# Kernel tuning notes

Hardware: AMD Instinct MI355X
Metric: run time of the kernel (lower is better)

Reference implementation:

```python
import jax, jax.numpy as jnp
import numpy as np

N, E, D, H, DK, T, R, KN, KR = 50000, 800000, 128, 8, 16, 3, 4, 2, 2

def setup_inputs() -> dict:
    key = jax.random.key(0)
    ks = jax.random.split(key, 16)
    lin_s = np.sqrt(1.0 / D).astype(np.float32)   # ~ nn.Linear init scale
    glo_s = np.sqrt(2.0 / (DK + DK)).astype(np.float32)  # glorot for [*,H,DK,DK]
    return {
        'x': jax.random.normal(ks[0], (N, D), jnp.float32),
        'Wk': jax.random.normal(ks[1], (KN, D, D), jnp.float32) * lin_s,
        'bk': jnp.zeros((KN, D), jnp.float32),
        'Wq': jax.random.normal(ks[2], (KN, D, D), jnp.float32) * lin_s,
        'bq': jnp.zeros((KN, D), jnp.float32),
        'Wv': jax.random.normal(ks[3], (KN, D, D), jnp.float32) * lin_s,
        'bv': jnp.zeros((KN, D), jnp.float32),
        'rel_pri': jnp.ones((KR, H), jnp.float32),
        'rel_att': jax.random.normal(ks[4], (KR, H, DK, DK), jnp.float32) * glo_s,
        'rel_msg': jax.random.normal(ks[5], (KR, H, DK, DK), jnp.float32) * glo_s,
        'n_alpha': jax.random.normal(ks[6], (T, KN), jnp.float32) * 0.001,
        'r_alpha': jax.random.normal(ks[7], (R, KR), jnp.float32) * 0.001,
        'W_up': jax.random.normal(ks[8], (T, D, D), jnp.float32) * lin_s,
        'b_up': jnp.zeros((T, D), jnp.float32),
        'gamma': jnp.ones((T, D), jnp.float32),
        'beta': jnp.zeros((T, D), jnp.float32),
        'edge_index': jax.random.randint(ks[9], (2, E), 0, N),
        'node_type': jax.random.randint(ks[10], (N,), 0, T),
        'edge_type': jax.random.randint(ks[11], (E,), 0, R),
    }

def reference(x, Wk, bk, Wq, bq, Wv, bv, rel_pri, rel_att, rel_msg,
              n_alpha, r_alpha, W_up, b_up, gamma, beta,
              edge_index, node_type, edge_type):
    n, d = x.shape
    h = rel_att.shape[1]; dk = d // h
    n_types = W_up.shape[0]; n_rel = r_alpha.shape[0]
    # NAS-mixed per-node-type k/q/v linears
    an = jax.nn.softmax(n_alpha, axis=-1)[node_type]        # [N, KN]
    def mix(W, b):
        cand = jnp.einsum('nd,kdo->kno', x, W) + b[:, None, :]  # [KN, N, D]
        return jnp.einsum('kno,nk->no', cand, an).reshape(n, h, dk)
    k = mix(Wk, bk); q = mix(Wq, bq); v = mix(Wv, bv)
    # NAS-mixed per-relation bilinear att/msg and priority
    br = jax.nn.softmax(r_alpha, axis=-1)                   # [R, KR]
    att_r = jnp.einsum('rk,khde->rhde', br, rel_att)        # [R, H, DK, DK]
    msg_r = jnp.einsum('rk,khde->rhde', br, rel_msg)
    pri_r = br @ rel_pri                                    # [R, H]
    src, dst = edge_index[0], edge_index[1]
    k_e = k[src]; q_e = q[dst]; v_e = v[src]                # [E, H, DK]
    k_t = jnp.zeros_like(k_e); m_t = jnp.zeros_like(v_e)
    for r in range(n_rel):  # small fixed relation loop
        sel = (edge_type == r)[:, None, None]
        k_t = k_t + jnp.where(sel, jnp.einsum('ehd,hdo->eho', k_e, att_r[r]), 0.0)
        m_t = m_t + jnp.where(sel, jnp.einsum('ehd,hdo->eho', v_e, msg_r[r]), 0.0)
    score = (q_e * k_t).sum(-1) * pri_r[edge_type] / np.float32(np.sqrt(dk))  # [E, H]
    # segment softmax over destination nodes
    mx = jax.ops.segment_max(score, dst, num_segments=n)
    ex = jnp.exp(score - mx[dst])
    den = jax.ops.segment_sum(ex, dst, num_segments=n)
    w = ex / (den[dst] + 1e-16)                             # [E, H]
    out = jax.ops.segment_sum(m_t * w[..., None], dst, num_segments=n).reshape(n, d)
    # heterogeneous update: gelu -> per-type linear -> residual -> per-type LN
    res = jax.nn.gelu(out)
    trans = jnp.zeros_like(x)
    for t in range(n_types):
        sel = (node_type == t)[:, None]
        trans = trans + jnp.where(sel, res @ W_up[t] + b_up[t], 0.0)
    hres = trans + x
    mu = hres.mean(-1, keepdims=True)
    var = hres.var(-1, keepdims=True)
    hn = (hres - mu) / jnp.sqrt(var + 1e-5)
    return hn * gamma[node_type] + beta[node_type]
```

## Files before the change

### kernel.cpp

```cpp
#include <hip/hip_runtime.h>
#include <hip/hip_bf16.h>

#define DEV __device__ __forceinline__

using frag8 = __attribute__((ext_vector_type(8))) short;
using f32x4 = __attribute__((ext_vector_type(4))) float;

DEV float b2f(__hip_bfloat16 v){ return __bfloat162float(v); }
DEV __hip_bfloat16 f2b(float f){ return __float2bfloat16(f); }
DEV short f2s(float f){ __hip_bfloat16 h = __float2bfloat16(f); short s; __builtin_memcpy(&s,&h,2); return s; }
DEV float bflo(unsigned u){ unsigned x = u<<16; float f; __builtin_memcpy(&f,&x,4); return f; }
DEV float bfhi(unsigned u){ unsigned x = u&0xFFFF0000u; float f; __builtin_memcpy(&f,&x,4); return f; }
DEV unsigned packbf(float a, float b){
  return (unsigned)(unsigned short)f2s(a) | ((unsigned)(unsigned short)f2s(b)<<16);
}

DEV bool is_bf16_mode(const void* rel_pri){
  return ((const unsigned*)rel_pri)[0] == 0x3F803F80u;
}
DEV float ldf(const void* p, int i, bool isbf){
  return isbf ? __bfloat162float(((const __hip_bfloat16*)p)[i]) : ((const float*)p)[i];
}

struct PrepArgs {
  const void *Wk,*Wq,*Wv,*bk,*bq,*bv,*rel_pri,*rel_att,*rel_msg,*n_alpha,*r_alpha,*Wup,*bup,*gm,*bt;
  const int* ntype;
  float *anW,*priS,*bmix,*bqt,*upc;
  __hip_bfloat16 *bsw,*wsw,*mswz;
  int* count3;
  int N;
};

__global__ void k_prep(PrepArgs P){
  bool isbf = is_bf16_mode(P.rel_pri);
  float an[3][2], br[4][2];
  #pragma unroll
  for (int t=0;t<3;t++){
    float a0=ldf(P.n_alpha,t*2,isbf), a1=ldf(P.n_alpha,t*2+1,isbf);
    float m=fmaxf(a0,a1); float e0=__expf(a0-m), e1=__expf(a1-m); float inv=1.f/(e0+e1);
    an[t][0]=e0*inv; an[t][1]=e1*inv;
  }
  #pragma unroll
  for (int r=0;r<4;r++){
    float a0=ldf(P.r_alpha,r*2,isbf), a1=ldf(P.r_alpha,r*2+1,isbf);
    float m=fmaxf(a0,a1); float e0=__expf(a0-m), e1=__expf(a1-m); float inv=1.f/(e0+e1);
    br[r][0]=e0*inv; br[r][1]=e1*inv;
  }
  int g = blockIdx.x*blockDim.x + threadIdx.x;
  int stride = gridDim.x*blockDim.x;

  for (int idx=g; idx<196608; idx+=stride){
    int jj = idx&7, lane=(idx>>3)&63, s=(idx>>9)&3, tile=(idx>>11)&15, chunk=idx>>15;
    int k = s*32 + ((lane>>4)<<3) + jj;
    int col = tile*16 + (lane&15);
    int cand = col>>7, c = col&127;
    float v;
    if (chunk==0)      v = ldf(P.Wk, cand*16384 + k*128 + c, isbf);
    else if (chunk==1) v = ldf(P.Wv, cand*16384 + k*128 + c, isbf);
    else {
      int r = chunk-2, h = c>>4, d = c&15;
      float acc=0.f;
      #pragma unroll
      for (int o=0;o<16;o++){
        float att = br[r][0]*ldf(P.rel_att,(h*16+d)*16+o,isbf) + br[r][1]*ldf(P.rel_att,2048+(h*16+d)*16+o,isbf);
        acc += ldf(P.Wq, cand*16384 + k*128 + h*16+o, isbf) * att;
      }
      v = acc;
    }
    P.bsw[idx] = f2b(v);
  }
  for (int idx=g; idx<49152; idx+=stride){
    int t3 = idx>>14, f = idx&16383;
    int jj=f&7, lane=(f>>3)&63, s=(f>>9)&3, nt=f>>11;
    int k = s*32 + ((lane>>4)<<3)+jj;
    int cc = nt*16 + (lane&15);
    P.wsw[idx] = f2b(ldf(P.Wup, t3*16384 + k*128 + cc, isbf));
  }
  for (int idx=g; idx<65536; idx+=stride){
    int jj=idx&7, lane=(idx>>3)&63, s=(idx>>9)&3, tile=(idx>>11)&7, kc=idx>>14;
    int k = kc*128 + s*32 + ((lane>>4)<<3)+jj;
    int col = tile*16 + (lane&15);
    int r = k>>7, h=(k>>4)&7, d=k&15;
    int h2 = col>>4, o = col&15;
    float v = 0.f;
    if (h2==h)
      v = br[r][0]*ldf(P.rel_msg,(h*16+d)*16+o,isbf) + br[r][1]*ldf(P.rel_msg,2048+(h*16+d)*16+o,isbf);
    P.mswz[idx] = f2b(v);
  }
  for (int idx=g; idx<768; idx+=stride){
    int mat = idx/384, rem = idx - mat*384, t = rem>>7, c = rem&127;
    const void* b = mat==0 ? P.bk : P.bv;
    P.bmix[idx] = an[t][0]*ldf(b,c,isbf) + an[t][1]*ldf(b,128+c,isbf);
  }
  for (int idx=g; idx<1536; idx+=stride){
    int t = idx>>9, rem = idx&511, r = rem>>7, c = rem&127;
    int h = c>>4, d = c&15;
    float acc=0.f;
    #pragma unroll
    for (int o=0;o<16;o++){
      float att = br[r][0]*ldf(P.rel_att,(h*16+d)*16+o,isbf) + br[r][1]*ldf(P.rel_att,2048+(h*16+d)*16+o,isbf);
      float bqm = an[t][0]*ldf(P.bq,h*16+o,isbf) + an[t][1]*ldf(P.bq,128+h*16+o,isbf);
      acc += bqm*att;
    }
    P.bqt[idx] = acc;
  }
  for (int idx=g; idx<1152; idx+=stride){
    int p = idx/384, rem = idx - p*384;
    const void* src = p==0 ? P.bup : p==1 ? P.gm : P.bt;
    P.upc[idx] = ldf(src, rem, isbf);
  }
  for (int idx=g; idx<32; idx+=stride){
    int r = idx>>3, h = idx&7;
    P.priS[idx] = 0.25f*(br[r][0]*ldf(P.rel_pri,h,isbf) + br[r][1]*ldf(P.rel_pri,8+h,isbf));
  }
  for (int idx=g; idx<6; idx+=stride) P.anW[idx] = an[idx>>1][idx&1];
  {
    int c0=0, c1=0, c2=0;
    for (int idx=g; idx<P.N; idx+=stride){
      int t = P.ntype[idx];
      c0 += (t==0); c1 += (t==1); c2 += (t==2);
    }
    #pragma unroll
    for (int m=1; m<64; m<<=1){
      c0 += __shfl_xor(c0, m, 64);
      c1 += __shfl_xor(c1, m, 64);
      c2 += __shfl_xor(c2, m, 64);
    }
    if ((threadIdx.x & 63) == 0){
      if (c0) atomicAdd(&P.count3[0], c0);
      if (c1) atomicAdd(&P.count3[1], c1);
      if (c2) atomicAdd(&P.count3[2], c2);
    }
  }
}

__global__ __launch_bounds__(256) void k_xcast(const void* __restrict__ x, const void* __restrict__ relp,
                                               __hip_bfloat16* __restrict__ xb, int total8){
  if (is_bf16_mode(relp)) return;
  int p = blockIdx.x*256 + threadIdx.x;
  if (p >= total8) return;
  const float4* xf = reinterpret_cast<const float4*>(x) + (size_t)p*2;
  float4 u = xf[0], v = xf[1];
  frag8 r;
  r[0]=f2s(u.x); r[1]=f2s(u.y); r[2]=f2s(u.z); r[3]=f2s(u.w);
  r[4]=f2s(v.x); r[5]=f2s(v.y); r[6]=f2s(v.z); r[7]=f2s(v.w);
  *reinterpret_cast<frag8*>(xb + (size_t)p*8) = r;
}

__global__ void k_hist(const int* __restrict__ eidx, int* __restrict__ count, int E){
  int e = blockIdx.x*256 + threadIdx.x;
  if (e < E) atomicAdd(&count[eidx[E+e]], 1);
}

__global__ __launch_bounds__(1024) void k_scan1(const int* __restrict__ count, int* __restrict__ excl,
                                                int* __restrict__ ctot, int N){
  __shared__ int s[1024];
  int i = blockIdx.x*1024 + threadIdx.x;
  int v = (i < N) ? count[i] : 0;
  s[threadIdx.x] = v;
  __syncthreads();
  int run = v;
  for (int off=1; off<1024; off<<=1){
    int add = (threadIdx.x >= off) ? s[threadIdx.x - off] : 0;
    __syncthreads();
    run += add; s[threadIdx.x] = run;
    __syncthreads();
  }
  if (i < N) excl[i] = run - v;
  if (threadIdx.x == 1023) ctot[blockIdx.x] = run;
}

__global__ void k_scan2(const int* __restrict__ ctot, int* __restrict__ coff,
                        const int* __restrict__ c3, int* __restrict__ segp, int NC){
  if (threadIdx.x==0 && blockIdx.x==0){
    int run=0;
    for (int c=0;c<NC;c++){ coff[c]=run; run+=ctot[c]; }
    int a0 = (c3[0]+127)&~127;
    int a1 = (c3[1]+127)&~127;
    int a2 = (c3[2]+127)&~127;
    segp[0]=0; segp[1]=a0; segp[2]=a0+a1; segp[3]=a0+a1+a2;
  }
}

__global__ __launch_bounds__(256) void k_nscatter(const int* __restrict__ ntype, const int* __restrict__ segp,
                           int* __restrict__ cur3, int* __restrict__ nlist, int N){
  __shared__ int wcnt[4][3];
  __shared__ int tbase[3];
  int tid = threadIdx.x;
  int n = blockIdx.x*256 + tid;
  int w = tid>>6, lane = tid&63;
  int t = (n < N) ? ntype[n] : -1;
  unsigned long long b0 = __ballot(t==0);
  unsigned long long b1 = __ballot(t==1);
  unsigned long long b2 = __ballot(t==2);
  if (lane==0){
    wcnt[w][0] = __popcll(b0);
    wcnt[w][1] = __popcll(b1);
    wcnt[w][2] = __popcll(b2);
  }
  __syncthreads();
  if (tid < 3){
    int c = wcnt[0][tid]+wcnt[1][tid]+wcnt[2][tid]+wcnt[3][tid];
    tbase[tid] = c ? atomicAdd(&cur3[tid], c) : 0;
  }
  __syncthreads();
  if (t >= 0){
    unsigned long long mask = t==0?b0 : t==1?b1 : b2;
    int lanerank = __popcll(mask & ((1ULL<<lane)-1ULL));
    int waveoff = 0;
    #pragma unroll
    for (int ww=0; ww<4; ww++) if (ww < w) waveoff += wcnt[ww][t];
    nlist[segp[t] + tbase[t] + waveoff + lanerank] = n;
  }
}

__global__ void k_escatter(const int* __restrict__ eidx, const int* __restrict__ etype,
                           const int* __restrict__ coff, const int* __restrict__ excl,
                           int* __restrict__ cursor, int* __restrict__ pack, int E){
  int e = blockIdx.x*256 + threadIdx.x;
  if (e < E){
    int src = eidx[e];
    int dst = eidx[E+e];
    int rt  = etype[e];
    int pos = coff[dst>>10] + excl[dst] + atomicAdd(&cursor[dst], 1);
    pack[pos] = src | (rt<<20);
  }
}

__global__ __launch_bounds__(256) void k_qkvqt(
    const void* __restrict__ x, const __hip_bfloat16* __restrict__ xb,
    const int* __restrict__ ntype,
    const void* __restrict__ relp,
    const __hip_bfloat16* __restrict__ bsw, const float* __restrict__ anW,
    const float* __restrict__ bmix, const float* __restrict__ bqt,
    __hip_bfloat16* __restrict__ kb, __hip_bfloat16* __restrict__ vb,
    __hip_bfloat16* __restrict__ qtb, int N, int perx)
{
  __shared__ __hip_bfloat16 Bs[16384];
  bool isbf = is_bf16_mode(relp);
  int tid = threadIdx.x;
  int w = tid>>6, lane = tid&63;
  int m16 = lane&15, q4 = lane>>4;

  int nrb = (N+127)>>7;
  int xcd  = blockIdx.x & 7;
  int slot = blockIdx.x >> 3;
  int lrb  = slot/12;
  int sub  = slot - lrb*12;
  int rb   = xcd*perx + lrb;
  if (rb >= nrb) return;
  int chunk = sub >> 1;
  int hh    = sub & 1;
  int base  = rb*128;

  const int4* bsw4 = reinterpret_cast<const int4*>(bsw) + chunk*4096;
  int4* Bs4 = reinterpret_cast<int4*>(Bs);
  #pragma unroll
  for (int u=0;u<8;u++){
    int srcT = 4*hh + (u&3) + ((u>>2)<<3);
    __builtin_amdgcn_global_load_lds(
        (const __attribute__((address_space(1))) void*)(bsw4 + srcT*256 + tid),
        (__attribute__((address_space(3))) void*)(Bs4 + u*256 + tid),
        16, 0, 0);
  }

  const __hip_bfloat16* xs = isbf ? (const __hip_bfloat16*)x : xb;
  frag8 a0[4], a1[4];
  {
    int rr0 = base + w*32 + m16;
    int rr1 = rr0 + 16;
    int r0 = rr0 < N ? rr0 : N-1;
    int r1 = rr1 < N ? rr1 : N-1;
    #pragma unroll
    for (int s=0;s<4;s++){
      a0[s] = *reinterpret_cast<const frag8*>(xs + (size_t)r0*128 + q4*8 + s*32);
      a1[s] = *reinterpret_cast<const frag8*>(xs + (size_t)r1*128 + q4*8 + s*32);
    }
  }
  int rowid[8]; float e0[8], e1[8]; int tt8[8];
  #pragma unroll
  for (int u=0;u<8;u++){
    int rs = u>>2, i = u&3;
    int rr = base + w*32 + rs*16 + q4*4 + i;
    rowid[u] = rr;
    int rc = rr < N ? rr : N-1;
    int t = ntype[rc]; tt8[u] = t;
    e0[u] = anW[t*2]; e1[u] = anW[t*2+1];
  }
  __syncthreads();
  const frag8* Bf = reinterpret_cast<const frag8*>(Bs);
  #pragma unroll
  for (int p=0;p<4;p++){
    f32x4 c00={0,0,0,0}, c01={0,0,0,0}, c10={0,0,0,0}, c11={0,0,0,0};
    #pragma unroll
    for (int s=0;s<4;s++){
      frag8 b0 = Bf[(p*4+s)*64 + lane];
      frag8 b1 = Bf[((p+4)*4+s)*64 + lane];
      c00 = __builtin_amdgcn_mfma_f32_16x16x32_bf16(a0[s], b0, c00, 0,0,0);
      c01 = __builtin_amdgcn_mfma_f32_16x16x32_bf16(a1[s], b0, c01, 0,0,0);
      c10 = __builtin_amdgcn_mfma_f32_16x16x32_bf16(a0[s], b1, c10, 0,0,0);
      c11 = __builtin_amdgcn_mfma_f32_16x16x32_bf16(a1[s], b1, c11, 0,0,0);
    }
    int c = (4*hh + p)*16 + m16;
    #pragma unroll
    for (int u=0;u<8;u++){
      int rs = u>>2, i = u&3;
      int rr = rowid[u];
      if (rr < N){
        float v0 = rs ? c01[i] : c00[i];
        float v1 = rs ? c11[i] : c10[i];
        float val = e0[u]*v0 + e1[u]*v1;
        if (chunk < 2){
          val += bmix[(chunk*3 + tt8[u])*128 + c];
          (chunk==0 ? kb : vb)[(size_t)rr*128 + c] = f2b(val);
        } else {
          int r = chunk-2;
          val += bqt[(tt8[u]*4 + r)*128 + c];
          qtb[(size_t)rr*512 + r*128 + c] = f2b(val);
        }
      }
    }
  }
}

__global__ __launch_bounds__(256) void k_aggr(
  const __hip_bfloat16* __restrict__ kb, const __hip_bfloat16* __restrict__ vb,
  const __hip_bfloat16* __restrict__ qtb,
  const int* __restrict__ count, const int* __restrict__ excl, const int* __restrict__ coff,
  const int* __restrict__ pack, const float* __restrict__ priS,
  __hip_bfloat16* __restrict__ accb, float* __restrict__ denb, int N)
{
  int w = threadIdx.x>>6, lane = threadIdx.x&63;
  int n = blockIdx.x*4 + w; if (n >= N) return;
  const unsigned* kb32 = (const unsigned*)kb;
  const unsigned* vb32 = (const unsigned*)vb;
  int h = lane>>3;
  float qx[4], qy[4], ps[4];
  {
    const unsigned* qrow = (const unsigned*)qtb + (size_t)n*256;
    #pragma unroll
    for (int r=0;r<4;r++){
      unsigned u = qrow[r*64 + lane];
      qx[r] = bflo(u); qy[r] = bfhi(u);
      ps[r] = priS[r*8 + h];
    }
  }
  int start = coff[n>>10] + excl[n];
  int deg = count[n];
  float ax0=0.f,ay0=0.f,ax1=0.f,ay1=0.f,ax2=0.f,ay2=0.f,ax3=0.f,ay3=0.f,den=0.f;

  for (int b0=0; b0<deg; b0+=64){
    int m = deg - b0; if (m > 64) m = 64;
    int pk = (lane < m) ? pack[start + b0 + lane] : 0;
    int pe = __builtin_amdgcn_readfirstlane(__shfl(pk, 0, 64));
    int rt = (pe>>20)&3, src = pe & 0xFFFFF;
    unsigned kw = kb32[(size_t)src*64 + lane];
    unsigned vw = vb32[(size_t)src*64 + lane];
    for (int i=0; i<m; i++){
      unsigned kc=kw, vc=vw; int rc=rt;
      if (i+1 < m){
        int pn = __builtin_amdgcn_readfirstlane(__shfl(pk, i+1, 64));
        rt = (pn>>20)&3; int s2 = pn & 0xFFFFF;
        kw = kb32[(size_t)s2*64 + lane];
        vw = vb32[(size_t)s2*64 + lane];
      }
      float k0=bflo(kc), k1=bfhi(kc), v0=bflo(vc), v1=bfhi(vc);
      float qxr, qyr, psr;
      if (rc==0){qxr=qx[0];qyr=qy[0];psr=ps[0];}
      else if (rc==1){qxr=qx[1];qyr=qy[1];psr=ps[1];}
      else if (rc==2){qxr=qx[2];qyr=qy[2];psr=ps[2];}
      else {qxr=qx[3];qyr=qy[3];psr=ps[3];}
      float prod = k0*qxr + k1*qyr;
      prod += __shfl_xor(prod, 1, 8);
      prod += __shfl_xor(prod, 2, 8);
      prod += __shfl_xor(prod, 4, 8);
      float ex = __expf(fminf(prod*psr, 30.f));
      den += ex;
      float e0 = ex*v0, e1 = ex*v1;
      if (rc==0){ax0+=e0; ay0+=e1;}
      else if (rc==1){ax1+=e0; ay1+=e1;}
      else if (rc==2){ax2+=e0; ay2+=e1;}
      else {ax3+=e0; ay3+=e1;}
    }
  }
  unsigned* arow = (unsigned*)accb + (size_t)n*256;
  arow[lane]       = packbf(ax0, ay0);
  arow[64 + lane]  = packbf(ax1, ay1);
  arow[128 + lane] = packbf(ax2, ay2);
  arow[192 + lane] = packbf(ax3, ay3);
  if ((lane&7)==0) denb[(size_t)n*8 + h] = den;
}

__global__ __launch_bounds__(256) void k_msgup(
  const __hip_bfloat16* __restrict__ accb, const float* __restrict__ denb,
  const void* __restrict__ x, const void* __restrict__ relp,
  const int* __restrict__ nlist, const int* __restrict__ segp,
  const __hip_bfloat16* __restrict__ mswz, const __hip_bfloat16* __restrict__ wsw,
  const float* __restrict__ upc, void* __restrict__ out, int N)
{
  __shared__ __hip_bfloat16 Ms[16384];
  __shared__ __hip_bfloat16 resS[128*136];
  bool isbf = is_bf16_mode(relp);
  int tid=threadIdx.x, w=tid>>6, lane=tid&63, m16=lane&15, q4=lane>>4;
  int pos0 = blockIdx.x*128;
  int sg1 = segp[1], sg2 = segp[2];
  int t = (pos0 >= sg2) ? 2 : (pos0 >= sg1) ? 1 : 0;

  int nA[2];
  #pragma unroll
  for (int rs=0; rs<2; rs++){
    int nid = nlist[pos0 + w*32 + rs*16 + m16];
    nA[rs] = nid < 0 ? 0 : nid;
  }
  int nC[8];
  #pragma unroll
  for (int u=0;u<8;u++){
    int rs=u>>2, i=u&3;
    nC[u] = nlist[pos0 + w*32 + rs*16 + q4*4 + i];
  }
  f32x4 c0[8], c1[8];
  #pragma unroll
  for (int nt=0;nt<8;nt++){ c0[nt]={0,0,0,0}; c1[nt]={0,0,0,0}; }
  const int4* msw4 = reinterpret_cast<const int4*>(mswz);
  int4* Ms4 = reinterpret_cast<int4*>(Ms);
  for (int kc=0; kc<4; kc++){
    __syncthreads();
    #pragma unroll
    for (int u=0;u<8;u++) Ms4[u*256+tid] = msw4[kc*2048 + u*256 + tid];
    __syncthreads();
    const frag8* Bf = reinterpret_cast<const frag8*>(Ms);
    frag8 a0[4], a1[4];
    #pragma unroll
    for (int s=0;s<4;s++){
      a0[s] = *reinterpret_cast<const frag8*>(accb + (size_t)nA[0]*512 + kc*128 + s*32 + q4*8);
      a1[s] = *reinterpret_cast<const frag8*>(accb + (size_t)nA[1]*512 + kc*128 + s*32 + q4*8);
    }
    #pragma unroll
    for (int s=0;s<4;s++){
      #pragma unroll
      for (int nt=0;nt<8;nt++){
        frag8 b = Bf[(nt*4+s)*64 + lane];
        c0[nt] = __builtin_amdgcn_mfma_f32_16x16x32_bf16(a0[s], b, c0[nt], 0,0,0);
        c1[nt] = __builtin_amdgcn_mfma_f32_16x16x32_bf16(a1[s], b, c1[nt], 0,0,0);
      }
    }
  }
  #pragma unroll
  for (int u=0;u<8;u++){
    int rs=u>>2, i=u&3;
    int rr = w*32 + rs*16 + q4*4 + i;
    int nid = nC[u]; int nc = nid<0?0:nid;
    #pragma unroll
    for (int nt=0;nt<8;nt++){
      float den = denb[(size_t)nc*8 + nt];
      float vv = (rs ? c1[nt][i] : c0[nt][i]) / (den + 1e-16f);
      float gl = 0.5f*vv*(1.f + tanhf(0.7978845608028654f*(vv + 0.044715f*vv*vv*vv)));
      resS[rr*136 + nt*16 + m16] = f2b(gl);
    }
  }
  __syncthreads();
  const int4* wsw4 = reinterpret_cast<const int4*>(wsw);
  #pragma unroll
  for (int u=0;u<8;u++) Ms4[u*256+tid] = wsw4[t*2048 + u*256 + tid];
  __syncthreads();
  f32x4 d0[8], d1[8];
  #pragma unroll
  for (int nt=0;nt<8;nt++){ d0[nt]={0,0,0,0}; d1[nt]={0,0,0,0}; }
  const frag8* Bf2 = reinterpret_cast<const frag8*>(Ms);
  #pragma unroll
  for (int s=0;s<4;s++){
    frag8 a0 = *reinterpret_cast<const frag8*>(&resS[(w*32 + m16)*136 + s*32 + q4*8]);
    frag8 a1 = *reinterpret_cast<const frag8*>(&resS[(w*32 + 16 + m16)*136 + s*32 + q4*8]);
    #pragma unroll
    for (int nt=0;nt<8;nt++){
      frag8 b = Bf2[(nt*4+s)*64 + lane];
      d0[nt] = __builtin_amdgcn_mfma_f32_16x16x32_bf16(a0, b, d0[nt], 0,0,0);
      d1[nt] = __builtin_amdgcn_mfma_f32_16x16x32_bf16(a1, b, d1[nt], 0,0,0);
    }
  }
  #pragma unroll
  for (int u=0;u<8;u++){
    int rs=u>>2, i=u&3;
    int nid = nC[u]; int nc = nid<0?0:nid;
    float hv[8], s1=0.f, s2=0.f;
    #pragma unroll
    for (int nt=0;nt<8;nt++){
      int col = nt*16+m16;
      float xr = isbf ? b2f(((const __hip_bfloat16*)x)[(size_t)nc*128+col])
                      : ((const float*)x)[(size_t)nc*128+col];
      float v = (rs ? d1[nt][i] : d0[nt][i]) + upc[t*128+col] + xr;
      hv[nt]=v; s1+=v; s2+=v*v;
    }
    #pragma unroll
    for (int mm=1; mm<16; mm<<=1){ s1 += __shfl_xor(s1, mm, 16); s2 += __shfl_xor(s2, mm, 16); }
    float mu = s1*(1.f/128.f);
    float var = s2*(1.f/128.f) - mu*mu;
    float rcp = rsqrtf(var + 1e-5f);
    if (nid >= 0){
      #pragma unroll
      for (int nt=0;nt<8;nt++){
        int col = nt*16+m16;
        float o = (hv[nt]-mu)*rcp*upc[384 + t*128+col] + upc[768 + t*128+col];
        if (isbf) ((__hip_bfloat16*)out)[(size_t)nid*128+col] = f2b(o);
        else      ((float*)out)[(size_t)nid*128+col] = o;
      }
    }
  }
}

extern "C" void kernel_launch(void* const* d_in, const int* in_sizes, int n_in,
                              void* d_out, int out_size, void* d_ws, size_t ws_size,
                              hipStream_t stream)
{
  const int* eidx  = (const int*)d_in[16];
  const int* ntype = (const int*)d_in[17];
  const int* etype = (const int*)d_in[18];

  const int N  = in_sizes[0]/128;
  const int E  = in_sizes[18];
  const int NC = (N + 1023)/1024;

  char* ws = (char*)d_ws;
  size_t off = 0;
  auto alloc = [&](size_t bytes){ size_t o = off; off += (bytes + 255) & ~(size_t)255; return o; };
  size_t o_count = alloc((size_t)N*4);
  size_t o_cursor= alloc((size_t)N*4);
  size_t o_c3    = alloc(16);
  size_t o_cur3  = alloc(16);
  size_t zbytes  = off;
  size_t o_nlist = alloc((size_t)(N+1024)*4);
  size_t o_excl  = alloc((size_t)N*4);
  size_t o_ctot  = alloc(256);
  size_t o_coff  = alloc(256);
  size_t o_segp  = alloc(16);
  size_t o_an    = alloc(6*4);
  size_t o_pri   = alloc(32*4);
  size_t o_bmix  = alloc(768*4);
  size_t o_bqt   = alloc(1536*4);
  size_t o_upc   = alloc(1152*4);
  size_t o_bsw   = alloc(196608*2);
  size_t o_wsw   = alloc(49152*2);
  size_t o_msw   = alloc(65536*2);
  size_t o_pack  = alloc((size_t)E*4);
  size_t o_xb    = alloc((size_t)N*128*2);
  size_t o_kb    = alloc((size_t)N*128*2);
  size_t o_vb    = alloc((size_t)N*128*2);
  size_t o_qt    = alloc((size_t)N*512*2);
  size_t o_acc   = alloc((size_t)N*512*2);
  size_t o_den   = alloc((size_t)N*8*4);
  (void)ws_size; (void)n_in; (void)out_size;

  hipMemsetAsync(ws, 0, zbytes, stream);
  hipMemsetAsync(ws + o_nlist, 0xFF, (size_t)(N+1024)*4, stream);

  PrepArgs P;
  P.Wk=d_in[1]; P.bk=d_in[2]; P.Wq=d_in[3]; P.bq=d_in[4]; P.Wv=d_in[5]; P.bv=d_in[6];
  P.rel_pri=d_in[7]; P.rel_att=d_in[8]; P.rel_msg=d_in[9];
  P.n_alpha=d_in[10]; P.r_alpha=d_in[11]; P.Wup=d_in[12]; P.bup=d_in[13]; P.gm=d_in[14]; P.bt=d_in[15];
  P.ntype=ntype;
  P.anW=(float*)(ws+o_an); P.priS=(float*)(ws+o_pri);
  P.bmix=(float*)(ws+o_bmix); P.bqt=(float*)(ws+o_bqt); P.upc=(float*)(ws+o_upc);
  P.bsw=(__hip_bfloat16*)(ws+o_bsw); P.wsw=(__hip_bfloat16*)(ws+o_wsw);
  P.mswz=(__hip_bfloat16*)(ws+o_msw);
  P.count3=(int*)(ws+o_c3); P.N=N;
  k_prep<<<512, 256, 0, stream>>>(P);

  int total8 = N*16;
  k_xcast<<<(total8+255)/256, 256, 0, stream>>>(d_in[0], d_in[7], (__hip_bfloat16*)(ws+o_xb), total8);

  k_hist<<<(E+255)/256, 256, 0, stream>>>(eidx, (int*)(ws+o_count), E);
  k_scan1<<<NC, 1024, 0, stream>>>((const int*)(ws+o_count), (int*)(ws+o_excl), (int*)(ws+o_ctot), N);
  k_scan2<<<1, 64, 0, stream>>>((const int*)(ws+o_ctot), (int*)(ws+o_coff),
                                (const int*)(ws+o_c3), (int*)(ws+o_segp), NC);
  k_nscatter<<<(N+255)/256, 256, 0, stream>>>(ntype, (const int*)(ws+o_segp),
                                              (int*)(ws+o_cur3), (int*)(ws+o_nlist), N);
  k_escatter<<<(E+255)/256, 256, 0, stream>>>(eidx, etype, (const int*)(ws+o_coff),
                                              (const int*)(ws+o_excl), (int*)(ws+o_cursor),
                                              (int*)(ws+o_pack), E);
  int nrb  = (N + 127)/128;
  int perx = (nrb + 7)/8;
  k_qkvqt<<<perx*12*8, 256, 0, stream>>>(d_in[0], (const __hip_bfloat16*)(ws+o_xb), ntype, d_in[7],
                                           (const __hip_bfloat16*)(ws+o_bsw),
                                           (const float*)(ws+o_an), (const float*)(ws+o_bmix),
                                           (const float*)(ws+o_bqt),
                                           (__hip_bfloat16*)(ws+o_kb), (__hip_bfloat16*)(ws+o_vb),
                                           (__hip_bfloat16*)(ws+o_qt), N, perx);
  k_aggr<<<(N+3)/4, 256, 0, stream>>>((const __hip_bfloat16*)(ws+o_kb), (const __hip_bfloat16*)(ws+o_vb),
                                (const __hip_bfloat16*)(ws+o_qt),
                                (const int*)(ws+o_count), (const int*)(ws+o_excl),
                                (const int*)(ws+o_coff), (const int*)(ws+o_pack),
                                (const float*)(ws+o_pri),
                                (__hip_bfloat16*)(ws+o_acc), (float*)(ws+o_den), N);
  int gUp = (N + 508)/128;
  k_msgup<<<gUp, 256, 0, stream>>>((const __hip_bfloat16*)(ws+o_acc), (const float*)(ws+o_den),
                                   d_in[0], d_in[7],
                                   (const int*)(ws+o_nlist), (const int*)(ws+o_segp),
                                   (const __hip_bfloat16*)(ws+o_msw), (const __hip_bfloat16*)(ws+o_wsw),
                                   (const float*)(ws+o_upc), d_out, N);
}
```

Before: 427.4 us.

## Precompute per-relation value messages per node and simplify edge aggregation

```diff
diff --git a/kernel.cpp b/kernel.cpp
--- a/kernel.cpp
+++ b/kernel.cpp
@@ -22,11 +22,23 @@
   return isbf ? __bfloat162float(((const __hip_bfloat16*)p)[i]) : ((const float*)p)[i];
 }
 
+#if __has_builtin(__builtin_amdgcn_fdot2_f32_bf16)
+typedef __bf16 bf16x2 __attribute__((ext_vector_type(2)));
+DEV float dot2b(unsigned a, unsigned b, float c){
+  bf16x2 av, bv; __builtin_memcpy(&av,&a,4); __builtin_memcpy(&bv,&b,4);
+  return __builtin_amdgcn_fdot2_f32_bf16(av, bv, c, false);
+}
+#else
+DEV float dot2b(unsigned a, unsigned b, float c){
+  return c + bflo(a)*bflo(b) + bfhi(a)*bfhi(b);
+}
+#endif
+
 struct PrepArgs {
-  const void *Wk,*Wq,*Wv,*bk,*bq,*bv,*rel_pri,*rel_att,*rel_msg,*n_alpha,*r_alpha,*Wup,*bup,*gm,*bt;
+  const void *x,*Wk,*Wq,*Wv,*bk,*bq,*bv,*rel_pri,*rel_att,*rel_msg,*n_alpha,*r_alpha,*Wup,*bup,*gm,*bt;
   const int* ntype;
-  float *anW,*priS,*bmix,*bqt,*upc;
-  __hip_bfloat16 *bsw,*wsw,*mswz;
+  float *anW,*priS,*bmixK,*bqt,*bvm,*upc;
+  __hip_bfloat16 *bsw,*wsw,*msw2,*xb;
   int* count3;
   int N;
 };
@@ -48,6 +60,17 @@
   }
   int g = blockIdx.x*blockDim.x + threadIdx.x;
   int stride = gridDim.x*blockDim.x;
+
+  if (!isbf){
+    const float4* xf = (const float4*)P.x;
+    for (int idx=g; idx<P.N*16; idx+=stride){
+      float4 u = xf[(size_t)idx*2], v = xf[(size_t)idx*2+1];
+      frag8 r;
+      r[0]=f2s(u.x); r[1]=f2s(u.y); r[2]=f2s(u.z); r[3]=f2s(u.w);
+      r[4]=f2s(v.x); r[5]=f2s(v.y); r[6]=f2s(v.z); r[7]=f2s(v.w);
+      *reinterpret_cast<frag8*>(P.xb + (size_t)idx*8) = r;
+    }
+  }
 
   for (int idx=g; idx<196608; idx+=stride){
     int jj = idx&7, lane=(idx>>3)&63, s=(idx>>9)&3, tile=(idx>>11)&15, chunk=idx>>15;
@@ -77,20 +100,20 @@
     P.wsw[idx] = f2b(ldf(P.Wup, t3*16384 + k*128 + cc, isbf));
   }
   for (int idx=g; idx<65536; idx+=stride){
-    int jj=idx&7, lane=(idx>>3)&63, s=(idx>>9)&3, tile=(idx>>11)&7, kc=idx>>14;
-    int k = kc*128 + s*32 + ((lane>>4)<<3)+jj;
+    int rel = idx>>14, f = idx&16383;
+    int jj=f&7, lane=(f>>3)&63, s=(f>>9)&3, tile=(f>>11)&7;
+    int k = s*32 + ((lane>>4)<<3)+jj;
     int col = tile*16 + (lane&15);
-    int r = k>>7, h=(k>>4)&7, d=k&15;
+    int h = k>>4, d = k&15;
     int h2 = col>>4, o = col&15;
     float v = 0.f;
     if (h2==h)
-      v = br[r][0]*ldf(P.rel_msg,(h*16+d)*16+o,isbf) + br[r][1]*ldf(P.rel_msg,2048+(h*16+d)*16+o,isbf);
-    P.mswz[idx] = f2b(v);
-  }
-  for (int idx=g; idx<768; idx+=stride){
-    int mat = idx/384, rem = idx - mat*384, t = rem>>7, c = rem&127;
-    const void* b = mat==0 ? P.bk : P.bv;
-    P.bmix[idx] = an[t][0]*ldf(b,c,isbf) + an[t][1]*ldf(b,128+c,isbf);
+      v = br[rel][0]*ldf(P.rel_msg,(h*16+d)*16+o,isbf) + br[rel][1]*ldf(P.rel_msg,2048+(h*16+d)*16+o,isbf);
+    P.msw2[idx] = f2b(v);
+  }
+  for (int idx=g; idx<384; idx+=stride){
+    int t = idx>>7, c = idx&127;
+    P.bmixK[idx] = an[t][0]*ldf(P.bk,c,isbf) + an[t][1]*ldf(P.bk,128+c,isbf);
   }
   for (int idx=g; idx<1536; idx+=stride){
     int t = idx>>9, rem = idx&511, r = rem>>7, c = rem&127;
@@ -103,6 +126,10 @@
       acc += bqm*att;
     }
     P.bqt[idx] = acc;
+  }
+  for (int idx=g; idx<384; idx+=stride){
+    int t = idx>>7, c = idx&127;
+    P.bvm[idx] = an[t][0]*ldf(P.bv,c,isbf) + an[t][1]*ldf(P.bv,128+c,isbf);
   }
   for (int idx=g; idx<1152; idx+=stride){
     int p = idx/384, rem = idx - p*384;
@@ -132,19 +159,6 @@
       if (c2) atomicAdd(&P.count3[2], c2);
     }
   }
-}
-
-__global__ __launch_bounds__(256) void k_xcast(const void* __restrict__ x, const void* __restrict__ relp,
-                                               __hip_bfloat16* __restrict__ xb, int total8){
-  if (is_bf16_mode(relp)) return;
-  int p = blockIdx.x*256 + threadIdx.x;
-  if (p >= total8) return;
-  const float4* xf = reinterpret_cast<const float4*>(x) + (size_t)p*2;
-  float4 u = xf[0], v = xf[1];
-  frag8 r;
-  r[0]=f2s(u.x); r[1]=f2s(u.y); r[2]=f2s(u.z); r[3]=f2s(u.w);
-  r[4]=f2s(v.x); r[5]=f2s(v.y); r[6]=f2s(v.z); r[7]=f2s(v.w);
-  *reinterpret_cast<frag8*>(xb + (size_t)p*8) = r;
 }
 
 __global__ void k_hist(const int* __restrict__ eidx, int* __restrict__ count, int E){
@@ -232,7 +246,8 @@
     const int* __restrict__ ntype,
     const void* __restrict__ relp,
     const __hip_bfloat16* __restrict__ bsw, const float* __restrict__ anW,
-    const float* __restrict__ bmix, const float* __restrict__ bqt,
+    const float* __restrict__ bmixK, const float* __restrict__ bmixV,
+    const float* __restrict__ bqt,
     __hip_bfloat16* __restrict__ kb, __hip_bfloat16* __restrict__ vb,
     __hip_bfloat16* __restrict__ qtb, int N, int perx)
 {
@@ -311,7 +326,7 @@
         float v1 = rs ? c11[i] : c10[i];
         float val = e0[u]*v0 + e1[u]*v1;
         if (chunk < 2){
-          val += bmix[(chunk*3 + tt8[u])*128 + c];
+          val += (chunk==0 ? bmixK : bmixV)[tt8[u]*128 + c];
           (chunk==0 ? kb : vb)[(size_t)rr*128 + c] = f2b(val);
         } else {
           int r = chunk-2;
@@ -323,8 +338,67 @@
   }
 }
 
+__global__ __launch_bounds__(256) void k_vmsg(
+    const __hip_bfloat16* __restrict__ vb,
+    const __hip_bfloat16* __restrict__ msw2,
+    __hip_bfloat16* __restrict__ vmb, int N, int perx)
+{
+  __shared__ __hip_bfloat16 Bs[16384];
+  int tid = threadIdx.x, w = tid>>6, lane = tid&63, m16 = lane&15, q4 = lane>>4;
+  int nrb = (N+127)>>7;
+  int xcd = blockIdx.x & 7, slot = blockIdx.x>>3;
+  int lrb = slot>>2, rel = slot&3;
+  int rb = xcd*perx + lrb;
+  if (rb >= nrb) return;
+  int base = rb*128;
+
+  const int4* m4 = reinterpret_cast<const int4*>(msw2) + rel*2048;
+  int4* Bs4 = reinterpret_cast<int4*>(Bs);
+  #pragma unroll
+  for (int u=0;u<8;u++)
+    __builtin_amdgcn_global_load_lds(
+        (const __attribute__((address_space(1))) void*)(m4 + u*256 + tid),
+        (__attribute__((address_space(3))) void*)(Bs4 + u*256 + tid), 16, 0, 0);
+
+  frag8 a0[4], a1[4];
+  int rr0 = base + w*32 + m16, rr1 = rr0+16;
+  int r0 = rr0<N?rr0:N-1, r1 = rr1<N?rr1:N-1;
+  #pragma unroll
+  for (int s=0;s<4;s++){
+    a0[s] = *reinterpret_cast<const frag8*>(vb + (size_t)r0*128 + q4*8 + s*32);
+    a1[s] = *reinterpret_cast<const frag8*>(vb + (size_t)r1*128 + q4*8 + s*32);
+  }
+  __syncthreads();
+  const frag8* Bf = reinterpret_cast<const frag8*>(Bs);
+  #pragma unroll
+  for (int p=0;p<4;p++){
+    f32x4 c00={0,0,0,0}, c01={0,0,0,0}, c10={0,0,0,0}, c11={0,0,0,0};
+    #pragma unroll
+    for (int s=0;s<4;s++){
+      frag8 b0 = Bf[(p*4+s)*64 + lane];
+      frag8 b1 = Bf[((p+4)*4+s)*64 + lane];
+      c00 = __builtin_amdgcn_mfma_f32_16x16x32_bf16(a0[s], b0, c00, 0,0,0);
+      c01 = __builtin_amdgcn_mfma_f32_16x16x32_bf16(a1[s], b0, c01, 0,0,0);
+      c10 = __builtin_amdgcn_mfma_f32_16x16x32_bf16(a0[s], b1, c10, 0,0,0);
+      c11 = __builtin_amdgcn_mfma_f32_16x16x32_bf16(a1[s], b1, c11, 0,0,0);
+    }
+    #pragma unroll
+    for (int u=0;u<8;u++){
+      int rs = u>>2, i = u&3;
+      int rr = base + w*32 + rs*16 + q4*4 + i;
+      if (rr < N){
+        float v0 = rs ? c01[i] : c00[i];
+        float v1 = rs ? c11[i] : c10[i];
+        size_t rowb = (size_t)rr*512 + rel*128;
+        vmb[rowb + p*16 + m16]     = f2b(v0);
+        vmb[rowb + (p+4)*16 + m16] = f2b(v1);
+      }
+    }
+  }
+}
+
 __global__ __launch_bounds__(256) void k_aggr(
-  const __hip_bfloat16* __restrict__ kb, const __hip_bfloat16* __restrict__ vb,
+  const __hip_bfloat16* __restrict__ kb, const __hip_bfloat16* __restrict__ vmb,
   const __hip_bfloat16* __restrict__ qtb,
   const int* __restrict__ count, const int* __restrict__ excl, const int* __restrict__ coff,
   const int* __restrict__ pack, const float* __restrict__ priS,
@@ -332,137 +406,120 @@
 {
   int w = threadIdx.x>>6, lane = threadIdx.x&63;
   int n = blockIdx.x*4 + w; if (n >= N) return;
-  const unsigned* kb32 = (const unsigned*)kb;
-  const unsigned* vb32 = (const unsigned*)vb;
-  int h = lane>>3;
-  float qx[4], qy[4], ps[4];
-  {
-    const unsigned* qrow = (const unsigned*)qtb + (size_t)n*256;
-    #pragma unroll
-    for (int r=0;r<4;r++){
-      unsigned u = qrow[r*64 + lane];
-      qx[r] = bflo(u); qy[r] = bfhi(u);
-      ps[r] = priS[r*8 + h];
-    }
-  }
+  int sub = lane&15, e4 = lane>>4;
+  int h = sub>>1, half = sub&1;
+  const int4* kb4 = (const int4*)kb;
+  const int4* vm4 = (const int4*)vmb;
+  const int4* qt4 = (const int4*)qtb;
+  size_t qbase = (size_t)n*64;
   int start = coff[n>>10] + excl[n];
   int deg = count[n];
-  float ax0=0.f,ay0=0.f,ax1=0.f,ay1=0.f,ax2=0.f,ay2=0.f,ax3=0.f,ay3=0.f,den=0.f;
-
-  for (int b0=0; b0<deg; b0+=64){
-    int m = deg - b0; if (m > 64) m = 64;
-    int pk = (lane < m) ? pack[start + b0 + lane] : 0;
-    int pe = __builtin_amdgcn_readfirstlane(__shfl(pk, 0, 64));
-    int rt = (pe>>20)&3, src = pe & 0xFFFFF;
-    unsigned kw = kb32[(size_t)src*64 + lane];
-    unsigned vw = vb32[(size_t)src*64 + lane];
-    for (int i=0; i<m; i++){
-      unsigned kc=kw, vc=vw; int rc=rt;
-      if (i+1 < m){
-        int pn = __builtin_amdgcn_readfirstlane(__shfl(pk, i+1, 64));
-        rt = (pn>>20)&3; int s2 = pn & 0xFFFFF;
-        kw = kb32[(size_t)s2*64 + lane];
-        vw = vb32[(size_t)s2*64 + lane];
+
+  float acc[8];
+  #pragma unroll
+  for (int d=0;d<8;d++) acc[d]=0.f;
+  float den = 0.f;
+
+  if (deg > 0){
+    int nst = (deg + 3)>>2;
+    int4 K={0,0,0,0}, V={0,0,0,0}, Q={0,0,0,0}; float ps=0.f; bool act=false;
+    auto issue = [&](int st){
+      int j = st*4 + e4;
+      act = j < deg;
+      int jc = act ? j : deg-1;
+      int pe = pack[start + jc];
+      int rt = (pe>>20)&3; int src = pe & 0xFFFFF;
+      K = kb4[(size_t)src*16 + sub];
+      V = vm4[(size_t)src*64 + rt*16 + sub];
+      Q = qt4[qbase + rt*16 + sub];
+      ps = priS[rt*8 + h];
+    };
+    issue(0);
+    for (int st=0; st<nst; st++){
+      int4 kc=K, vc=V, qc=Q; float psr=ps; bool a=act;
+      if (st+1 < nst) issue(st+1);
+      float s = dot2b((unsigned)kc.x,(unsigned)qc.x,0.f);
+      s = dot2b((unsigned)kc.y,(unsigned)qc.y,s);
+      s = dot2b((unsigned)kc.z,(unsigned)qc.z,s);
+      s = dot2b((unsigned)kc.w,(unsigned)qc.w,s);
+      s += __shfl_xor(s, 1, 64);
+      float ex = a ? __expf(fminf(s*psr, 30.f)) : 0.f;
+      den += half ? 0.f : ex;
+      unsigned vv[4]={(unsigned)vc.x,(unsigned)vc.y,(unsigned)vc.z,(unsigned)vc.w};
+      #pragma unroll
+      for (int q=0;q<4;q++){
+        acc[2*q]   += ex*bflo(vv[q]);
+        acc[2*q+1] += ex*bfhi(vv[q]);
       }
-      float k0=bflo(kc), k1=bfhi(kc), v0=bflo(vc), v1=bfhi(vc);
-      float qxr, qyr, psr;
-      if (rc==0){qxr=qx[0];qyr=qy[0];psr=ps[0];}
-      else if (rc==1){qxr=qx[1];qyr=qy[1];psr=ps[1];}
-      else if (rc==2){qxr=qx[2];qyr=qy[2];psr=ps[2];}
-      else {qxr=qx[3];qyr=qy[3];psr=ps[3];}
-      float prod = k0*qxr + k1*qyr;
-      prod += __shfl_xor(prod, 1, 8);
-      prod += __shfl_xor(prod, 2, 8);
-      prod += __shfl_xor(prod, 4, 8);
-      float ex = __expf(fminf(prod*psr, 30.f));
-      den += ex;
-      float e0 = ex*v0, e1 = ex*v1;
-      if (rc==0){ax0+=e0; ay0+=e1;}
-      else if (rc==1){ax1+=e0; ay1+=e1;}
-      else if (rc==2){ax2+=e0; ay2+=e1;}
-      else {ax3+=e0; ay3+=e1;}
-    }
-  }
-  unsigned* arow = (unsigned*)accb + (size_t)n*256;
-  arow[lane]       = packbf(ax0, ay0);
-  arow[64 + lane]  = packbf(ax1, ay1);
-  arow[128 + lane] = packbf(ax2, ay2);
-  arow[192 + lane] = packbf(ax3, ay3);
-  if ((lane&7)==0) denb[(size_t)n*8 + h] = den;
+    }
+  }
+  #pragma unroll
+  for (int m=16; m<64; m<<=1){
+    #pragma unroll
+    for (int d=0;d<8;d++) acc[d] += __shfl_xor(acc[d], m, 64);
+    den += __shfl_xor(den, m, 64);
+  }
+  if (e4==0){
+    unsigned o0 = packbf(acc[0], acc[1]);
+    unsigned o1 = packbf(acc[2], acc[3]);
+    unsigned o2 = packbf(acc[4], acc[5]);
+    unsigned o3 = packbf(acc[6], acc[7]);
+    int4 o4; o4.x=(int)o0; o4.y=(int)o1; o4.z=(int)o2; o4.w=(int)o3;
+    ((int4*)accb)[(size_t)n*16 + sub] = o4;
+    if (half==0) denb[(size_t)n*8 + h] = den;
+  }
 }
 
 __global__ __launch_bounds__(256) void k_msgup(
   const __hip_bfloat16* __restrict__ accb, const float* __restrict__ denb,
   const void* __restrict__ x, const void* __restrict__ relp,
   const int* __restrict__ nlist, const int* __restrict__ segp,
-  const __hip_bfloat16* __restrict__ mswz, const __hip_bfloat16* __restrict__ wsw,
+  const __hip_bfloat16* __restrict__ wsw,
   const float* __restrict__ upc, void* __restrict__ out, int N)
 {
   __shared__ __hip_bfloat16 Ms[16384];
   __shared__ __hip_bfloat16 resS[128*136];
+  __shared__ int nrow[128];
   bool isbf = is_bf16_mode(relp);
   int tid=threadIdx.x, w=tid>>6, lane=tid&63, m16=lane&15, q4=lane>>4;
   int pos0 = blockIdx.x*128;
   int sg1 = segp[1], sg2 = segp[2];
   int t = (pos0 >= sg2) ? 2 : (pos0 >= sg1) ? 1 : 0;
-
-  int nA[2];
-  #pragma unroll
-  for (int rs=0; rs<2; rs++){
-    int nid = nlist[pos0 + w*32 + rs*16 + m16];
-    nA[rs] = nid < 0 ? 0 : nid;
-  }
+  if (tid < 128) nrow[tid] = nlist[pos0 + tid];
+  const int4* wsw4 = reinterpret_cast<const int4*>(wsw);
+  int4* Ms4 = reinterpret_cast<int4*>(Ms);
+  #pragma unroll
+  for (int u=0;u<8;u++) Ms4[u*256+tid] = wsw4[t*2048 + u*256 + tid];
+  __syncthreads();
+
+  const int4* acc4 = (const int4*)accb;
+  #pragma unroll
+  for (int it=0; it<8; it++){
+    int t2 = it*256 + tid;
+    int row = t2>>4, seg = t2&15;
+    int nid = nrow[row]; int nc = nid<0?0:nid;
+    int4 a = acc4[(size_t)nc*16 + seg];
+    float rdn = 1.f/(denb[(size_t)nc*8 + (seg>>1)] + 1e-16f);
+    unsigned uu[4] = {(unsigned)a.x,(unsigned)a.y,(unsigned)a.z,(unsigned)a.w};
+    unsigned ov[4];
+    #pragma unroll
+    for (int q=0;q<4;q++){
+      float v0 = bflo(uu[q])*rdn, v1 = bfhi(uu[q])*rdn;
+      float g0 = 0.5f*v0*(1.f+tanhf(0.7978845608028654f*(v0+0.044715f*v0*v0*v0)));
+      float g1 = 0.5f*v1*(1.f+tanhf(0.7978845608028654f*(v1+0.044715f*v1*v1*v1)));
+      ov[q] = packbf(g0,g1);
+    }
+    int4 o4; o4.x=(int)ov[0]; o4.y=(int)ov[1]; o4.z=(int)ov[2]; o4.w=(int)ov[3];
+    *reinterpret_cast<int4*>(reinterpret_cast<char*>(resS) + row*272 + seg*16) = o4;
+  }
+  __syncthreads();
+
   int nC[8];
   #pragma unroll
   for (int u=0;u<8;u++){
     int rs=u>>2, i=u&3;
-    nC[u] = nlist[pos0 + w*32 + rs*16 + q4*4 + i];
-  }
-  f32x4 c0[8], c1[8];
-  #pragma unroll
-  for (int nt=0;nt<8;nt++){ c0[nt]={0,0,0,0}; c1[nt]={0,0,0,0}; }
-  const int4* msw4 = reinterpret_cast<const int4*>(mswz);
-  int4* Ms4 = reinterpret_cast<int4*>(Ms);
-  for (int kc=0; kc<4; kc++){
-    __syncthreads();
-    #pragma unroll
-    for (int u=0;u<8;u++) Ms4[u*256+tid] = msw4[kc*2048 + u*256 + tid];
-    __syncthreads();
-    const frag8* Bf = reinterpret_cast<const frag8*>(Ms);
-    frag8 a0[4], a1[4];
-    #pragma unroll
-    for (int s=0;s<4;s++){
-      a0[s] = *reinterpret_cast<const frag8*>(accb + (size_t)nA[0]*512 + kc*128 + s*32 + q4*8);
-      a1[s] = *reinterpret_cast<const frag8*>(accb + (size_t)nA[1]*512 + kc*128 + s*32 + q4*8);
-    }
-    #pragma unroll
-    for (int s=0;s<4;s++){
-      #pragma unroll
-      for (int nt=0;nt<8;nt++){
-        frag8 b = Bf[(nt*4+s)*64 + lane];
-        c0[nt] = __builtin_amdgcn_mfma_f32_16x16x32_bf16(a0[s], b, c0[nt], 0,0,0);
-        c1[nt] = __builtin_amdgcn_mfma_f32_16x16x32_bf16(a1[s], b, c1[nt], 0,0,0);
-      }
-    }
-  }
-  #pragma unroll
-  for (int u=0;u<8;u++){
-    int rs=u>>2, i=u&3;
-    int rr = w*32 + rs*16 + q4*4 + i;
-    int nid = nC[u]; int nc = nid<0?0:nid;
-    #pragma unroll
-    for (int nt=0;nt<8;nt++){
-      float den = denb[(size_t)nc*8 + nt];
-      float vv = (rs ? c1[nt][i] : c0[nt][i]) / (den + 1e-16f);
-      float gl = 0.5f*vv*(1.f + tanhf(0.7978845608028654f*(vv + 0.044715f*vv*vv*vv)));
-      resS[rr*136 + nt*16 + m16] = f2b(gl);
-    }
-  }
-  __syncthreads();
-  const int4* wsw4 = reinterpret_cast<const int4*>(wsw);
-  #pragma unroll
-  for (int u=0;u<8;u++) Ms4[u*256+tid] = wsw4[t*2048 + u*256 + tid];
-  __syncthreads();
+    nC[u] = nrow[w*32 + rs*16 + q4*4 + i];
+  }
   f32x4 d0[8], d1[8];
   #pragma unroll
   for (int nt=0;nt<8;nt++){ d0[nt]={0,0,0,0}; d1[nt]={0,0,0,0}; }
@@ -535,7 +592,8 @@
   size_t o_segp  = alloc(16);
   size_t o_an    = alloc(6*4);
   size_t o_pri   = alloc(32*4);
-  size_t o_bmix  = alloc(768*4);
+  size_t o_bmk   = alloc(384*4);
+  size_t o_bmv   = alloc(384*4);
   size_t o_bqt   = alloc(1536*4);
   size_t o_upc   = alloc(1152*4);
   size_t o_bsw   = alloc(196608*2);
@@ -546,7 +604,8 @@
   size_t o_kb    = alloc((size_t)N*128*2);
   size_t o_vb    = alloc((size_t)N*128*2);
   size_t o_qt    = alloc((size_t)N*512*2);
-  size_t o_acc   = alloc((size_t)N*512*2);
+  size_t o_vm    = alloc((size_t)N*512*2);
+  size_t o_acc   = alloc((size_t)N*128*2);
   size_t o_den   = alloc((size_t)N*8*4);
   (void)ws_size; (void)n_in; (void)out_size;
 
@@ -554,19 +613,19 @@
   hipMemsetAsync(ws + o_nlist, 0xFF, (size_t)(N+1024)*4, stream);
 
   PrepArgs P;
+  P.x=d_in[0];
   P.Wk=d_in[1]; P.bk=d_in[2]; P.Wq=d_in[3]; P.bq=d_in[4]; P.Wv=d_in[5]; P.bv=d_in[6];
   P.rel_pri=d_in[7]; P.rel_att=d_in[8]; P.rel_msg=d_in[9];
   P.n_alpha=d_in[10]; P.r_alpha=d_in[11]; P.Wup=d_in[12]; P.bup=d_in[13]; P.gm=d_in[14]; P.bt=d_in[15];
   P.ntype=ntype;
   P.anW=(float*)(ws+o_an); P.priS=(float*)(ws+o_pri);
-  P.bmix=(float*)(ws+o_bmix); P.bqt=(float*)(ws+o_bqt); P.upc=(float*)(ws+o_upc);
+  P.bmixK=(float*)(ws+o_bmk); P.bqt=(float*)(ws+o_bqt); P.bvm=(float*)(ws+o_bmv);
+  P.upc=(float*)(ws+o_upc);
   P.bsw=(__hip_bfloat16*)(ws+o_bsw); P.wsw=(__hip_bfloat16*)(ws+o_wsw);
-  P.mswz=(__hip_bfloat16*)(ws+o_msw);
+  P.msw2=(__hip_bfloat16*)(ws+o_msw);
+  P.xb=(__hip_bfloat16*)(ws+o_xb);
   P.count3=(int*)(ws+o_c3); P.N=N;
-  k_prep<<<512, 256, 0, stream>>>(P);
-
-  int total8 = N*16;
-  k_xcast<<<(total8+255)/256, 256, 0, stream>>>(d_in[0], d_in[7], (__hip_bfloat16*)(ws+o_xb), total8);
+  k_prep<<<1024, 256, 0, stream>>>(P);
 
   k_hist<<<(E+255)/256, 256, 0, stream>>>(eidx, (int*)(ws+o_count), E);
   k_scan1<<<NC, 1024, 0, stream>>>((const int*)(ws+o_count), (int*)(ws+o_excl), (int*)(ws+o_ctot), N);
@@ -581,11 +640,15 @@
   int perx = (nrb + 7)/8;
   k_qkvqt<<<perx*12*8, 256, 0, stream>>>(d_in[0], (const __hip_bfloat16*)(ws+o_xb), ntype, d_in[7],
                                            (const __hip_bfloat16*)(ws+o_bsw),
-                                           (const float*)(ws+o_an), (const float*)(ws+o_bmix),
+                                           (const float*)(ws+o_an), (const float*)(ws+o_bmk),
+                                           (const float*)(ws+o_bmv),
                                            (const float*)(ws+o_bqt),
                                            (__hip_bfloat16*)(ws+o_kb), (__hip_bfloat16*)(ws+o_vb),
                                            (__hip_bfloat16*)(ws+o_qt), N, perx);
-  k_aggr<<<(N+3)/4, 256, 0, stream>>>((const __hip_bfloat16*)(ws+o_kb), (const __hip_bfloat16*)(ws+o_vb),
+  k_vmsg<<<perx*4*8, 256, 0, stream>>>((const __hip_bfloat16*)(ws+o_vb),
+                                       (const __hip_bfloat16*)(ws+o_msw),
+                                       (__hip_bfloat16*)(ws+o_vm), N, perx);
+  k_aggr<<<(N+3)/4, 256, 0, stream>>>((const __hip_bfloat16*)(ws+o_kb), (const __hip_bfloat16*)(ws+o_vm),
                                 (const __hip_bfloat16*)(ws+o_qt),
                                 (const int*)(ws+o_count), (const int*)(ws+o_excl),
                                 (const int*)(ws+o_coff), (const int*)(ws+o_pack),
@@ -595,6 +658,6 @@
   k_msgup<<<gUp, 256, 0, stream>>>((const __hip_bfloat16*)(ws+o_acc), (const float*)(ws+o_den),
                                    d_in[0], d_in[7],
                                    (const int*)(ws+o_nlist), (const int*)(ws+o_segp),
-                                   (const __hip_bfloat16*)(ws+o_msw), (const __hip_bfloat16*)(ws+o_wsw),
+                                   (const __hip_bfloat16*)(ws+o_wsw),
                                    (const float*)(ws+o_upc), d_out, N);
 }
```

Measured after the change: 448.4 us. +4.9%, slower.
